# Kernel tuning notes

Measured on AMD Instinct MI355X. Metric: run time of the kernel, lower is better.

## Reference

```python
import jax, jax.numpy as jnp
import numpy as np

K = 4
G = 64
IN_DIM = 256
OUT_DIM = 256
BATCH = 512
T0, T1 = -1.0, 1.0


def setup_inputs() -> dict:
    key = jax.random.key(0)
    kx, kw = jax.random.split(key)
    x = jax.random.uniform(kx, (BATCH, IN_DIM), jnp.float32, T0, T1)
    # xavier_normal_ on [G+K, in, out]: std = sqrt(2 / (fan_in + fan_out)) with fan over last two dims
    std = (2.0 / (IN_DIM + OUT_DIM)) ** 0.5
    w = jax.random.normal(kw, (G + K, IN_DIM, OUT_DIM), jnp.float32) * std
    # knot vector: k-1 repeats of t0, linspace(t0,t1,G+1), k-1 repeats of t1
    t = jnp.concatenate([
        jnp.full((K - 1,), T0, jnp.float32),
        jnp.linspace(T0, T1, G + 1, dtype=jnp.float32),
        jnp.full((K - 1,), T1, jnp.float32),
    ])
    return {"x": x, "w": w, "t": t, "k": K}


def _basis(x, t, k):
    """Cox-de Boor: the k nonzero order-k B-spline basis values at each x.
    Returns (idx, N): idx [..., k] basis indices i-k+1..i, N [..., k] values."""
    n_t = t.shape[0]
    # interval i with t[i] <= x < t[i+1], clipped to the valid span
    i = jnp.clip(jnp.searchsorted(t, x, side='right') - 1, k - 1, n_t - k - 1)
    N = jnp.ones(x.shape + (1,), x.dtype)
    for p in range(1, k):  # static small loop (k=4)
        jj = jnp.arange(1, p + 1)
        left = x[..., None] - t[i[..., None] + 1 - jj]   # [..., p]
        right = t[i[..., None] + jj] - x[..., None]      # [..., p]
        saved = jnp.zeros_like(x)
        vals = []
        for r in range(p):
            d = right[..., r] + left[..., p - 1 - r]      # t[i+r+1] - t[i+r+1-p]
            temp = N[..., r] / d
            vals.append(saved + right[..., r] * temp)
            saved = left[..., p - 1 - r] * temp
        vals.append(saved)
        N = jnp.stack(vals, -1)
    idx = i[..., None] - (k - 1) + jnp.arange(k)
    return idx, N


def reference(x, w, t, k):
    in_dim = x.shape[1]
    n_rows = w.shape[0]
    idx, y1 = _basis(x, t, k)                             # [B,in,k], [B,in,k]
    # last row of w (index -1 == n_rows-1) weights the SiLU residual term
    idx_full = jnp.concatenate(
        [idx, jnp.full(idx.shape[:-1] + (1,), n_rows - 1, idx.dtype)], -1)  # [B,in,k+1]
    silu = x * jax.nn.sigmoid(x)
    y2 = jnp.concatenate([y1, silu[..., None]], -1)       # [B,in,k+1]
    # gather local spline coefficients: w2[b,c,j,o] = w[idx_full[b,c,j], c, o]
    w2 = w[idx_full, jnp.arange(in_dim)[None, :, None], :]  # [B,in,k+1,out]
    return jnp.einsum('bcjo,bcj->bo', w2, y2)             # [B,out]
```

## Files before the change

kernel.cpp:

```cpp
#include <hip/hip_runtime.h>
#include <math.h>
#include <stdint.h>

#define IN_DIM  256
#define OUT_DIM 256
#define NROWS   68
#define NT      71
#define BATCH   512
#define W_ELEMS (NROWS * IN_DIM * OUT_DIM)
#define PART_FLOATS (4 * BATCH * OUT_DIM)

__device__ __forceinline__ uint32_t bf16_rne(float f) {
  uint32_t u = __builtin_bit_cast(uint32_t, f);
  return (u + 0x7fffu + ((u >> 16) & 1u)) >> 16;
}

__global__ __launch_bounds__(256) void cvt_kernel(const float* __restrict__ w,
                                                  uint32_t* __restrict__ wb) {
  const int base = (blockIdx.x * 256 + threadIdx.x) * 8;
  const float4 a = *(const float4*)(w + base);
  const float4 b = *(const float4*)(w + base + 4);
  uint4 o;
  o.x = bf16_rne(a.x) | (bf16_rne(a.y) << 16);
  o.y = bf16_rne(a.z) | (bf16_rne(a.w) << 16);
  o.z = bf16_rne(b.x) | (bf16_rne(b.y) << 16);
  o.w = bf16_rne(b.z) | (bf16_rne(b.w) << 16);
  *(uint4*)(wb + base / 2) = o;
}

__device__ __forceinline__ void fma8(const uint4 q, const float y, float* acc) {
  acc[0] += y * __builtin_bit_cast(float, q.x << 16);
  acc[1] += y * __builtin_bit_cast(float, q.x & 0xffff0000u);
  acc[2] += y * __builtin_bit_cast(float, q.y << 16);
  acc[3] += y * __builtin_bit_cast(float, q.y & 0xffff0000u);
  acc[4] += y * __builtin_bit_cast(float, q.z << 16);
  acc[5] += y * __builtin_bit_cast(float, q.z & 0xffff0000u);
  acc[6] += y * __builtin_bit_cast(float, q.w << 16);
  acc[7] += y * __builtin_bit_cast(float, q.w & 0xffff0000u);
}

__global__ __launch_bounds__(256) void kan_gather_kernel(
    const float* __restrict__ x, const uint4* __restrict__ wp,
    const float* __restrict__ t, float* __restrict__ part) {
  __shared__ float  lt[NT];
  __shared__ float4 lyv[64];
  __shared__ float  lys[64];
  __shared__ int    lbase[64];
  __shared__ float  red[8 * 32 * 9];

  const int tid = threadIdx.x;
  const unsigned bid = blockIdx.x;
  const int sl = (bid & 7) >> 1;
  const int b  = ((bid & 1) << 8) | (bid >> 3);

  if (tid < NT) lt[tid] = t[tid];
  __syncthreads();

  if (tid < 64) {
    const int c = sl * 64 + tid;
    const float xv = x[b * IN_DIM + c];
    int i = 3 + (int)floorf((xv + 1.0f) * 32.0f);
    i = i < 3 ? 3 : (i > 66 ? 66 : i);
    while (i > 3 && xv < lt[i]) --i;
    while (i < 66 && xv >= lt[i + 1]) ++i;

    float N0 = 1.f, N1 = 0.f, N2 = 0.f, N3 = 0.f;
    {
      const float l1 = xv - lt[i];
      const float r1 = lt[i + 1] - xv;
      const float tp = N0 / (r1 + l1);
      N1 = l1 * tp; N0 = r1 * tp;
    }
    {
      const float l1 = xv - lt[i];
      const float l2 = xv - lt[i - 1];
      const float r1 = lt[i + 1] - xv;
      const float r2 = lt[i + 2] - xv;
      float saved = 0.f;
      const float tp0 = N0 / (r1 + l2);
      const float n0 = saved + r1 * tp0; saved = l2 * tp0;
      const float tp1 = N1 / (r2 + l1);
      const float n1 = saved + r2 * tp1; saved = l1 * tp1;
      N0 = n0; N1 = n1; N2 = saved;
    }
    {
      const float l1 = xv - lt[i];
      const float l2 = xv - lt[i - 1];
      const float l3 = xv - lt[i - 2];
      const float r1 = lt[i + 1] - xv;
      const float r2 = lt[i + 2] - xv;
      const float r3 = lt[i + 3] - xv;
      float saved = 0.f;
      const float tp0 = N0 / (r1 + l3);
      const float n0 = saved + r1 * tp0; saved = l3 * tp0;
      const float tp1 = N1 / (r2 + l2);
      const float n1 = saved + r2 * tp1; saved = l2 * tp1;
      const float tp2 = N2 / (r3 + l1);
      const float n2 = saved + r3 * tp2; saved = l1 * tp2;
      N0 = n0; N1 = n1; N2 = n2; N3 = saved;
    }
    lyv[tid]   = make_float4(N0, N1, N2, N3);
    lys[tid]   = xv / (1.0f + expf(-xv));
    lbase[tid] = i - 3;
  }
  __syncthreads();

  const int ol = tid & 31;
  const int cs = tid >> 5;

  float acc[8] = {0.f, 0.f, 0.f, 0.f, 0.f, 0.f, 0.f, 0.f};
  const int cbeg = cs * 8;
  #pragma unroll 2
  for (int m = 0; m < 8; ++m) {
    const int cl = cbeg + m;
    const float4 yv = lyv[cl];
    const float  ys = lys[cl];
    const int base  = lbase[cl];
    const uint4* p  = wp + (size_t)(sl * 64 + cl) * 32 + ol;
    const uint4 q0 = p[(size_t)(base + 0) * 8192];
    const uint4 q1 = p[(size_t)(base + 1) * 8192];
    const uint4 q2 = p[(size_t)(base + 2) * 8192];
    const uint4 q3 = p[(size_t)(base + 3) * 8192];
    const uint4 q4 = p[(size_t)67 * 8192];
    fma8(q0, yv.x, acc);
    fma8(q1, yv.y, acc);
    fma8(q2, yv.z, acc);
    fma8(q3, yv.w, acc);
    fma8(q4, ys,   acc);
  }

  float* r = &red[(cs * 32 + ol) * 9];
  #pragma unroll
  for (int j = 0; j < 8; ++j) r[j] = acc[j];
  __syncthreads();
  if (tid < 64) {
    const int olr = tid >> 1;
    const int jb  = (tid & 1) * 4;
    float4 s = make_float4(0.f, 0.f, 0.f, 0.f);
    #pragma unroll
    for (int sI = 0; sI < 8; ++sI) {
      const float* rr = &red[(sI * 32 + olr) * 9 + jb];
      s.x += rr[0]; s.y += rr[1]; s.z += rr[2]; s.w += rr[3];
    }
    ((float4*)(part + ((size_t)sl * BATCH + b) * OUT_DIM))[tid] = s;
  }
}

__global__ __launch_bounds__(256) void reduce_kernel(const float* __restrict__ part,
                                                     float* __restrict__ out) {
  const int q = blockIdx.x * 256 + threadIdx.x;
  const float4* p0 = (const float4*)(part);
  const float4* p1 = (const float4*)(part + BATCH * OUT_DIM);
  const float4* p2 = (const float4*)(part + 2 * BATCH * OUT_DIM);
  const float4* p3 = (const float4*)(part + 3 * BATCH * OUT_DIM);
  const float4 a = p0[q], b = p1[q], c = p2[q], d = p3[q];
  float4 s;
  s.x = (a.x + b.x) + (c.x + d.x);
  s.y = (a.y + b.y) + (c.y + d.y);
  s.z = (a.z + b.z) + (c.z + d.z);
  s.w = (a.w + b.w) + (c.w + d.w);
  ((float4*)out)[q] = s;
}

extern "C" void kernel_launch(void* const* d_in, const int* in_sizes, int n_in,
                              void* d_out, int out_size, void* d_ws, size_t ws_size,
                              hipStream_t stream) {
  const float* x = (const float*)d_in[0];
  const float* w = (const float*)d_in[1];
  const float* t = (const float*)d_in[2];
  float* out  = (float*)d_out;
  float* part = (float*)d_ws;
  uint32_t* wb = (uint32_t*)d_ws + PART_FLOATS;
  cvt_kernel<<<W_ELEMS / (256 * 8), 256, 0, stream>>>(w, wb);
  kan_gather_kernel<<<BATCH * 4, 256, 0, stream>>>(x, (const uint4*)wb, t, part);
  reduce_kernel<<<BATCH * OUT_DIM / 4 / 256, 256, 0, stream>>>(part, out);
}
```

Measured before the change: 90.35 us.

## Process 8 batch rows per block over 32-channel chunks to reuse SiLU weights

The gather kernel now gives each block 8 batch rows and a 32-input-channel chunk, where before each block handled one row and a 64-channel slice. The SiLU weight row is then loaded once and reused across the 8 rows, each thread keeps 64 accumulators, and the two half-waves are combined with a cross-lane shuffle before a shared-memory reduction. The grid shrinks from 2048 to 512 blocks and the partial buffer grows to 8 slices, so the final reduce kernel reads twice as much data. In exchange, register pressure and lower occupancy may reduce latency hiding for the random gathers.

```diff
diff --git a/kernel.cpp b/kernel.cpp
--- a/kernel.cpp
+++ b/kernel.cpp
@@ -8,7 +8,7 @@
 #define NT      71
 #define BATCH   512
 #define W_ELEMS (NROWS * IN_DIM * OUT_DIM)
-#define PART_FLOATS (4 * BATCH * OUT_DIM)
+#define PART_FLOATS (8 * BATCH * OUT_DIM)
 
 __device__ __forceinline__ uint32_t bf16_rne(float f) {
   uint32_t u = __builtin_bit_cast(uint32_t, f);
@@ -43,22 +43,23 @@
     const float* __restrict__ x, const uint4* __restrict__ wp,
     const float* __restrict__ t, float* __restrict__ part) {
   __shared__ float  lt[NT];
-  __shared__ float4 lyv[64];
-  __shared__ float  lys[64];
-  __shared__ int    lbase[64];
-  __shared__ float  red[8 * 32 * 9];
+  __shared__ float4 nA[32][8];
+  __shared__ float  sA[32][8];
+  __shared__ int    bA[32][8];
+  __shared__ float  red[4][2048];
 
   const int tid = threadIdx.x;
   const unsigned bid = blockIdx.x;
-  const int sl = (bid & 7) >> 1;
-  const int b  = ((bid & 1) << 8) | (bid >> 3);
+  const int cchunk = bid & 7;
+  const int bgroup = bid >> 3;
 
   if (tid < NT) lt[tid] = t[tid];
   __syncthreads();
 
-  if (tid < 64) {
-    const int c = sl * 64 + tid;
-    const float xv = x[b * IN_DIM + c];
+  {
+    const int bb = tid >> 5;
+    const int cl = tid & 31;
+    const float xv = x[(size_t)(bgroup * 8 + bb) * IN_DIM + cchunk * 32 + cl];
     int i = 3 + (int)floorf((xv + 1.0f) * 32.0f);
     i = i < 3 ? 3 : (i > 66 ? 66 : i);
     while (i > 3 && xv < lt[i]) --i;
@@ -99,66 +100,91 @@
       const float n2 = saved + r3 * tp2; saved = l1 * tp2;
       N0 = n0; N1 = n1; N2 = n2; N3 = saved;
     }
-    lyv[tid]   = make_float4(N0, N1, N2, N3);
-    lys[tid]   = xv / (1.0f + expf(-xv));
-    lbase[tid] = i - 3;
+    nA[cl][bb] = make_float4(N0, N1, N2, N3);
+    sA[cl][bb] = xv / (1.0f + expf(-xv));
+    bA[cl][bb] = i - 3;
   }
   __syncthreads();
 
-  const int ol = tid & 31;
-  const int cs = tid >> 5;
-
-  float acc[8] = {0.f, 0.f, 0.f, 0.f, 0.f, 0.f, 0.f, 0.f};
-  const int cbeg = cs * 8;
-  #pragma unroll 2
-  for (int m = 0; m < 8; ++m) {
-    const int cl = cbeg + m;
-    const float4 yv = lyv[cl];
-    const float  ys = lys[cl];
-    const int base  = lbase[cl];
-    const uint4* p  = wp + (size_t)(sl * 64 + cl) * 32 + ol;
-    const uint4 q0 = p[(size_t)(base + 0) * 8192];
-    const uint4 q1 = p[(size_t)(base + 1) * 8192];
-    const uint4 q2 = p[(size_t)(base + 2) * 8192];
-    const uint4 q3 = p[(size_t)(base + 3) * 8192];
-    const uint4 q4 = p[(size_t)67 * 8192];
-    fma8(q0, yv.x, acc);
-    fma8(q1, yv.y, acc);
-    fma8(q2, yv.z, acc);
-    fma8(q3, yv.w, acc);
-    fma8(q4, ys,   acc);
-  }
-
-  float* r = &red[(cs * 32 + ol) * 9];
+  const int wv   = tid >> 6;
+  const int lane = tid & 63;
+  const int half = lane >> 5;
+  const int ol   = lane & 31;
+
+  float acc[8][8];
   #pragma unroll
-  for (int j = 0; j < 8; ++j) r[j] = acc[j];
+  for (int b = 0; b < 8; ++b) {
+    #pragma unroll
+    for (int j = 0; j < 8; ++j) acc[b][j] = 0.f;
+  }
+
+  for (int pp = 0; pp < 4; ++pp) {
+    const int cl = wv * 8 + pp * 2 + half;
+    const uint32_t cbase = (uint32_t)((cchunk * 32 + cl) * 32 + ol);
+    const uint4 q4 = wp[cbase + 67u * 8192u];
+    #pragma unroll
+    for (int b = 0; b < 8; ++b) {
+      const float4 yv = nA[cl][b];
+      const float  ys = sA[cl][b];
+      const uint32_t rb = cbase + ((uint32_t)bA[cl][b] << 13);
+      const uint4 q0 = wp[rb];
+      const uint4 q1 = wp[rb +  8192u];
+      const uint4 q2 = wp[rb + 16384u];
+      const uint4 q3 = wp[rb + 24576u];
+      fma8(q0, yv.x, acc[b]);
+      fma8(q1, yv.y, acc[b]);
+      fma8(q2, yv.z, acc[b]);
+      fma8(q3, yv.w, acc[b]);
+      fma8(q4, ys,   acc[b]);
+    }
+  }
+
+  #pragma unroll
+  for (int b = 0; b < 8; ++b) {
+    #pragma unroll
+    for (int j = 0; j < 8; ++j)
+      acc[b][j] += __shfl_xor(acc[b][j], 32, 64);
+  }
+
+  if (half == 0) {
+    #pragma unroll
+    for (int b = 0; b < 8; ++b) {
+      #pragma unroll
+      for (int j = 0; j < 8; ++j)
+        red[wv][b * 256 + ol * 8 + j] = acc[b][j];
+    }
+  }
   __syncthreads();
-  if (tid < 64) {
-    const int olr = tid >> 1;
-    const int jb  = (tid & 1) * 4;
-    float4 s = make_float4(0.f, 0.f, 0.f, 0.f);
-    #pragma unroll
-    for (int sI = 0; sI < 8; ++sI) {
-      const float* rr = &red[(sI * 32 + olr) * 9 + jb];
-      s.x += rr[0]; s.y += rr[1]; s.z += rr[2]; s.w += rr[3];
-    }
-    ((float4*)(part + ((size_t)sl * BATCH + b) * OUT_DIM))[tid] = s;
+
+  {
+    const int b  = tid >> 5;
+    const int oo = tid & 31;
+    float4 s0 = make_float4(0.f, 0.f, 0.f, 0.f);
+    float4 s1 = make_float4(0.f, 0.f, 0.f, 0.f);
+    #pragma unroll
+    for (int w2 = 0; w2 < 4; ++w2) {
+      const float4 a0 = *(const float4*)&red[w2][b * 256 + oo * 8];
+      const float4 a1 = *(const float4*)&red[w2][b * 256 + oo * 8 + 4];
+      s0.x += a0.x; s0.y += a0.y; s0.z += a0.z; s0.w += a0.w;
+      s1.x += a1.x; s1.y += a1.y; s1.z += a1.z; s1.w += a1.w;
+    }
+    float* dst = part + ((size_t)cchunk * BATCH + bgroup * 8 + b) * OUT_DIM + oo * 8;
+    *(float4*)dst       = s0;
+    *(float4*)(dst + 4) = s1;
   }
 }
 
 __global__ __launch_bounds__(256) void reduce_kernel(const float* __restrict__ part,
                                                      float* __restrict__ out) {
   const int q = blockIdx.x * 256 + threadIdx.x;
-  const float4* p0 = (const float4*)(part);
-  const float4* p1 = (const float4*)(part + BATCH * OUT_DIM);
-  const float4* p2 = (const float4*)(part + 2 * BATCH * OUT_DIM);
-  const float4* p3 = (const float4*)(part + 3 * BATCH * OUT_DIM);
-  const float4 a = p0[q], b = p1[q], c = p2[q], d = p3[q];
-  float4 s;
-  s.x = (a.x + b.x) + (c.x + d.x);
-  s.y = (a.y + b.y) + (c.y + d.y);
-  s.z = (a.z + b.z) + (c.z + d.z);
-  s.w = (a.w + b.w) + (c.w + d.w);
+  const int S = BATCH * OUT_DIM / 4;
+  const float4* p = (const float4*)part;
+  float4 s = p[q];
+  #pragma unroll
+  for (int k = 1; k < 8; ++k) {
+    const float4 a = p[q + k * S];
+    s.x += a.x; s.y += a.y; s.z += a.z; s.w += a.w;
+  }
   ((float4*)out)[q] = s;
 }
 
@@ -172,6 +198,6 @@
   float* part = (float*)d_ws;
   uint32_t* wb = (uint32_t*)d_ws + PART_FLOATS;
   cvt_kernel<<<W_ELEMS / (256 * 8), 256, 0, stream>>>(w, wb);
-  kan_gather_kernel<<<BATCH * 4, 256, 0, stream>>>(x, (const uint4*)wb, t, part);
+  kan_gather_kernel<<<512, 256, 0, stream>>>(x, (const uint4*)wb, t, part);
   reduce_kernel<<<BATCH * OUT_DIM / 4 / 256, 256, 0, stream>>>(part, out);
 }
```

Result: no change. 89.77 us (-0.6%).
